# Kernel tuning notes

Hardware: AMD Instinct MI355X
Metric: run time of the kernel (lower is better)

## Reference

```python
import jax, jax.numpy as jnp
import numpy as np

# --- VMO muscle parameters (reconstructed VMOParameters defaults) ---
L0 = 0.089          # optimal_fiber_length [m]
LTS = 0.126         # tendon_slack_length [m]
PENN0 = 0.0873      # pennation_angle_at_optimal [rad]
VMAX = 10.0         # max contraction velocity [optimal lengths / s]
AF = 0.25           # Hill force-velocity curvature
FAT_RATE = 0.01     # fatigue_rate
REC_RATE = 0.002    # recovery_rate
TAU_ACT = 0.01      # activation time constant [s]
TAU_DEACT = 0.04    # deactivation time constant [s]
PHYSICS_WEIGHT = 0.8
LMT_DEFAULT = LTS + L0 * float(np.cos(PENN0))  # default_musculotendon_length
LMIN = 0.5 * L0
LMAX = 1.6 * L0
KT = 35.0           # tendon exponential stiffness
CT = 0.2            # tendon force scale

B, T, H = 8192, 2048, 64


def physics_rhs(state, exc):
    # state: [B, 3] = (fiber_length, activation, fatigue); exc: [B]
    lM = jnp.clip(state[..., 0], LMIN, LMAX)
    act = jnp.clip(state[..., 1], 0.01, 1.0)
    fat = jnp.clip(state[..., 2], 0.0, 1.0)
    a_eff = act * (1.0 - fat)
    # constant-thickness pennation model
    sin_p = jnp.clip(L0 * float(np.sin(PENN0)) / lM, 0.0, 0.99)
    cos_p = jnp.sqrt(1.0 - sin_p * sin_p)
    # Hill-type fiber velocity ODE (elastic tendon, lMT fixed at default, vMT = 0)
    lT = LMT_DEFAULT - lM * cos_p
    epsT = (lT - LTS) / LTS
    fT = jnp.where(epsT > 0.0, CT * (jnp.exp(KT * epsT) - 1.0), 0.0)
    lN = lM / L0
    fL = jnp.exp(-((lN - 1.0) ** 2) / 0.45)
    fPE = jnp.where(lN > 1.0,
                    (jnp.exp(5.0 * (lN - 1.0) / 0.6) - 1.0) / (float(np.exp(5.0)) - 1.0),
                    0.0)
    fV = (fT / cos_p - fPE) / (a_eff * fL + 1e-3)
    vN = jnp.clip((fV - 1.0) / (1.0 + jnp.abs(fV) / AF), -1.0, 1.5)  # inverse force-velocity
    fiber_velocity = VMAX * L0 * vN
    # first-order activation dynamics with activation-dependent time constant
    tau = jnp.where(exc > act, TAU_ACT * (0.5 + 1.5 * act), TAU_DEACT / (0.5 + 1.5 * act))
    activation_dot = (exc - act) / tau
    fatigue_dot = FAT_RATE * a_eff * (1.0 - fat) - REC_RATE * (1.0 - a_eff) * fat
    return jnp.stack([fiber_velocity, activation_dot, fatigue_dot], axis=-1)


def neural_correction(state, exc, W1, b1, W2, b2, W3, b3):
    x = jnp.concatenate([state, exc[..., None]], axis=-1)  # [B, 4]
    h = jnp.tanh(x @ W1 + b1)
    h = jnp.tanh(h @ W2 + b2)
    return 0.1 * jnp.tanh(h @ W3 + b3)


def ode_forward(initial_state, excitation_signal, t_span, W1, b1, W2, b2, W3, b3):
    n = t_span.shape[0]

    def rhs(t, y):
        # piecewise-constant excitation: torch.bucketize(t, t_span) - 1, clamped
        idx = jnp.clip(jnp.searchsorted(t_span, t, side='left') - 1, 0, n - 1)
        exc = excitation_signal[:, idx]
        return physics_rhs(y, exc) + (1.0 - PHYSICS_WEIGHT) * neural_correction(
            y, exc, W1, b1, W2, b2, W3, b3)

    @jax.checkpoint
    def step(y, i):
        t0, t1 = t_span[i], t_span[i + 1]
        dt = t1 - t0
        k1 = rhs(t0, y)
        k2 = rhs(t0 + 0.5 * dt, y + 0.5 * dt * k1)
        k3 = rhs(t0 + 0.5 * dt, y + 0.5 * dt * k2)
        k4 = rhs(t1, y + dt * k3)
        y1 = y + (dt / 6.0) * (k1 + 2.0 * k2 + 2.0 * k3 + k4)
        return y1, y1

    _, ys = jax.lax.scan(step, initial_state, jnp.arange(n - 1))
    return jnp.concatenate([initial_state[None], ys], axis=0)  # [T, B, 3]


def setup_inputs() -> dict:
    key = jax.random.key(0)
    ks = jax.random.split(key, 6)
    lM0 = L0 * (0.8 + 0.4 * jax.random.uniform(ks[0], (B,)))
    a0 = 0.05 + 0.1 * jax.random.uniform(ks[1], (B,))
    initial_state = jnp.stack([lM0, a0, jnp.zeros((B,))], axis=-1).astype(jnp.float32)
    excitation_signal = jax.random.uniform(ks[2], (B, T), dtype=jnp.float32)
    t_span = jnp.linspace(0.0, 2.0, T, dtype=jnp.float32)
    s = 0.1
    W1 = s * jax.random.normal(ks[3], (4, H), dtype=jnp.float32)
    W2 = s * jax.random.normal(ks[4], (H, H), dtype=jnp.float32)
    W3 = s * jax.random.normal(ks[5], (H, 3), dtype=jnp.float32)
    b1 = jnp.zeros((H,), jnp.float32)
    b2 = jnp.zeros((H,), jnp.float32)
    b3 = jnp.zeros((3,), jnp.float32)
    return {"initial_state": initial_state, "excitation_signal": excitation_signal,
            "t_span": t_span, "W1": W1, "b1": b1, "W2": W2, "b2": b2, "W3": W3, "b3": b3}


def reference(initial_state, excitation_signal, t_span, W1, b1, W2, b2, W3, b3):
    return ode_forward(initial_state, excitation_signal, t_span, W1, b1, W2, b2, W3, b3)
```

## Files before the change

kernel.cpp:

```cpp
#include <hip/hip_runtime.h>
#include <cstdint>

#define B_SZ 8192
#define T_SZ 2048

#define C_LTS       0.126f
#define C_LMIN      (0.5f * 0.089f)
#define C_LMAX      (1.6f * 0.089f)
#define C_KT        35.0f
#define C_CT        0.2f
#define C_VMAX_L0   (10.0f * 0.089f)
#define C_AF_INV    4.0f
#define C_FAT_RATE  0.01f
#define C_REC_RATE  0.002f
#define C_TAU_ACT   0.01f
#define C_TAU_DEACT 0.04f
#define C_L0SIN     0.0077598346f
#define C_LMT_DEF   0.2146610680f
#define C_INV_EM5   0.006783655f
#define C_INV_LTS   (1.0f / 0.126f)
#define C_INV_L0    (1.0f / 0.089f)
#define C_NN_SCALE  0.02f

typedef __attribute__((ext_vector_type(8))) short bf16x8;
typedef __attribute__((ext_vector_type(4))) float f32x4;

__device__ __forceinline__ float fast_rcp(float x) { return __builtin_amdgcn_rcpf(x); }
__device__ __forceinline__ float fast_rsq(float x) { return __builtin_amdgcn_rsqf(x); }
__device__ __forceinline__ float fast_tanh(float x) {
    const float e2 = __expf(2.0f * x);
    return 1.0f - 2.0f * fast_rcp(e2 + 1.0f);
}
__device__ __forceinline__ float clampf(float x, float lo, float hi) {
    return fminf(fmaxf(x, lo), hi);
}
__device__ __forceinline__ short f2bf_trunc(float f) {
    return (short)(__float_as_uint(f) >> 16);
}
__device__ __forceinline__ short f2bf_rne(float f) {
    uint32_t u = __float_as_uint(f);
    u += 0x7fff + ((u >> 16) & 1);
    return (short)(u >> 16);
}
__device__ __forceinline__ float bf2f(short s) {
    return __uint_as_float(((uint32_t)(unsigned short)s) << 16);
}

__global__ __launch_bounds__(256) void ode_kernel(
    const float* __restrict__ init_state,
    const float* __restrict__ exc,
    const float* __restrict__ tspan,
    const float* __restrict__ W1,
    const float* __restrict__ b1,
    const float* __restrict__ W2,
    const float* __restrict__ b2,
    const float* __restrict__ W3,
    const float* __restrict__ b3,
    float* __restrict__ out)
{
    const int tid  = threadIdx.x;
    const int wv   = tid >> 6;
    const int lane = tid & 63;
    const int r    = lane & 15;
    const int q    = lane >> 4;
    const int el   = (blockIdx.x << 4) + r;

    __shared__ __align__(16) short h1hi[1024];
    __shared__ __align__(16) short h1lo[1024];
    __shared__ __align__(16) float psum[256];

    float w1r[4][4], b1r[4];
    {
        const int j0 = (wv << 4) + (q << 2);
        #pragma unroll
        for (int u = 0; u < 4; ++u) {
            const int j = j0 + u;
            b1r[u]   = b1[j];
            w1r[0][u] = W1[j];
            w1r[1][u] = W1[64 + j];
            w1r[2][u] = W1[128 + j];
            w1r[3][u] = W1[192 + j];
        }
    }
    const int col = (wv << 4) + r;
    bf16x8 Wh[2], Wl[2];
    #pragma unroll
    for (int ks = 0; ks < 2; ++ks)
        #pragma unroll
        for (int t = 0; t < 8; ++t) {
            const int k = (ks << 5) + (q << 3) + t;
            const float wgt = W2[(k << 6) + col];
            const short hi = f2bf_trunc(wgt);
            Wh[ks][t] = hi;
            Wl[ks][t] = f2bf_rne(wgt - bf2f(hi));
        }
    float b2v4[4], w3r[4][3];
    #pragma unroll
    for (int reg = 0; reg < 4; ++reg) {
        const int c = (wv << 4) + (q << 2) + reg;
        b2v4[reg]  = b2[c];
        w3r[reg][0] = W3[c * 3 + 0];
        w3r[reg][1] = W3[c * 3 + 1];
        w3r[reg][2] = W3[c * 3 + 2];
    }
    const float b3v0 = b3[0], b3v1 = b3[1], b3v2 = b3[2];

    const int slotW = (wv << 1) + (q >> 1);
    const int widx  = (r << 6) + ((slotW ^ (r & 7)) << 3) + ((q & 1) << 2);
    const int ridx0 = (r << 6) + ((q       ^ (r & 7)) << 3);
    const int ridx1 = (r << 6) + (((4 | q) ^ (r & 7)) << 3);
    const int pswidx = (wv << 6) + (r << 2);

    float yb0 = init_state[el * 3 + 0];
    float yb1 = init_state[el * 3 + 1];
    float yb2 = init_state[el * 3 + 2];
    float cs0 = yb0, cs1 = yb1, cs2 = yb2;
    float ka0 = 0.f, ka1 = 0.f, ka2 = 0.f;

    if (wv == 0 && q == 0) {
        out[(size_t)el * 3 + 0] = yb0;
        out[(size_t)el * 3 + 1] = yb1;
        out[(size_t)el * 3 + 2] = yb2;
    }

    const float* excp = exc + (size_t)el * T_SZ;
    float excB = excp[0];
    float excA = excB;
    float tA = tspan[0], tB = tspan[1];

    #pragma unroll 1
    for (int i = 0; i < T_SZ - 1; ++i) {
        const float excN = excp[(i < T_SZ - 2) ? (i + 1) : (T_SZ - 2)];
        const float tN   = tspan[(i <= T_SZ - 3) ? (i + 2) : (T_SZ - 1)];
        const float dt  = tB - tA;
        const float hdt = 0.5f * dt;

        #pragma unroll
        for (int ev = 0; ev < 4; ++ev) {
            const float excv = (ev == 0) ? excA : excB;
            const float s0 = cs0, s1 = cs1, s2 = cs2;

            uint32_t hi01, hi23, lo01, lo23;
            {
                float hv[4];
                #pragma unroll
                for (int u = 0; u < 4; ++u) {
                    float pre = b1r[u];
                    pre = fmaf(s0,   w1r[0][u], pre);
                    pre = fmaf(s1,   w1r[1][u], pre);
                    pre = fmaf(s2,   w1r[2][u], pre);
                    pre = fmaf(excv, w1r[3][u], pre);
                    hv[u] = fast_tanh(pre);
                }
                const unsigned short h0 = (unsigned short)f2bf_trunc(hv[0]);
                const unsigned short h1_ = (unsigned short)f2bf_trunc(hv[1]);
                const unsigned short h2_ = (unsigned short)f2bf_trunc(hv[2]);
                const unsigned short h3_ = (unsigned short)f2bf_trunc(hv[3]);
                hi01 = (uint32_t)h0 | ((uint32_t)h1_ << 16);
                hi23 = (uint32_t)h2_ | ((uint32_t)h3_ << 16);
                const unsigned short l0 = (unsigned short)f2bf_rne(hv[0] - bf2f((short)h0));
                const unsigned short l1 = (unsigned short)f2bf_rne(hv[1] - bf2f((short)h1_));
                const unsigned short l2 = (unsigned short)f2bf_rne(hv[2] - bf2f((short)h2_));
                const unsigned short l3 = (unsigned short)f2bf_rne(hv[3] - bf2f((short)h3_));
                lo01 = (uint32_t)l0 | ((uint32_t)l1 << 16);
                lo23 = (uint32_t)l2 | ((uint32_t)l3 << 16);
            }
            *reinterpret_cast<uint2*>(&h1hi[widx]) = make_uint2(hi01, hi23);
            *reinterpret_cast<uint2*>(&h1lo[widx]) = make_uint2(lo01, lo23);
            __syncthreads();

            const bf16x8 Hh0 = *reinterpret_cast<const bf16x8*>(&h1hi[ridx0]);
            const bf16x8 Hh1 = *reinterpret_cast<const bf16x8*>(&h1hi[ridx1]);
            const bf16x8 Hl0 = *reinterpret_cast<const bf16x8*>(&h1lo[ridx0]);
            const bf16x8 Hl1 = *reinterpret_cast<const bf16x8*>(&h1lo[ridx1]);

            f32x4 accA = {b2v4[0], b2v4[1], b2v4[2], b2v4[3]};
            f32x4 accB = {0.f, 0.f, 0.f, 0.f};
            accA = __builtin_amdgcn_mfma_f32_16x16x32_bf16(Wh[0], Hl0, accA, 0, 0, 0);
            accB = __builtin_amdgcn_mfma_f32_16x16x32_bf16(Wh[1], Hl1, accB, 0, 0, 0);
            accA = __builtin_amdgcn_mfma_f32_16x16x32_bf16(Wl[0], Hh0, accA, 0, 0, 0);
            accB = __builtin_amdgcn_mfma_f32_16x16x32_bf16(Wl[1], Hh1, accB, 0, 0, 0);
            accA = __builtin_amdgcn_mfma_f32_16x16x32_bf16(Wh[0], Hh0, accA, 0, 0, 0);
            accB = __builtin_amdgcn_mfma_f32_16x16x32_bf16(Wh[1], Hh1, accB, 0, 0, 0);

            float p0 = 0.f, p1 = 0.f, p2 = 0.f;
            #pragma unroll
            for (int reg = 0; reg < 4; ++reg) {
                const float h2v = fast_tanh(accA[reg] + accB[reg]);
                p0 = fmaf(h2v, w3r[reg][0], p0);
                p1 = fmaf(h2v, w3r[reg][1], p1);
                p2 = fmaf(h2v, w3r[reg][2], p2);
            }
            p0 += __shfl_xor(p0, 16, 64);
            p1 += __shfl_xor(p1, 16, 64);
            p2 += __shfl_xor(p2, 16, 64);
            p0 += __shfl_xor(p0, 32, 64);
            p1 += __shfl_xor(p1, 32, 64);
            p2 += __shfl_xor(p2, 32, 64);
            if (q == 0) {
                *reinterpret_cast<f32x4*>(&psum[pswidx]) = (f32x4){p0, p1, p2, p2};
            }
            __syncthreads();

            const f32x4 v0 = *reinterpret_cast<const f32x4*>(&psum[(r << 2)]);
            const f32x4 v1 = *reinterpret_cast<const f32x4*>(&psum[64 + (r << 2)]);
            const f32x4 v2 = *reinterpret_cast<const f32x4*>(&psum[128 + (r << 2)]);
            const f32x4 v3 = *reinterpret_cast<const f32x4*>(&psum[192 + (r << 2)]);
            const float S0 = (v0[0] + v1[0]) + (v2[0] + v3[0]);
            const float S1 = (v0[1] + v1[1]) + (v2[1] + v3[1]);
            const float S2 = (v0[2] + v1[2]) + (v2[2] + v3[2]);

            const float nn0 = C_NN_SCALE * fast_tanh(S0 + b3v0);
            const float nn1 = C_NN_SCALE * fast_tanh(S1 + b3v1);
            const float nn2 = C_NN_SCALE * fast_tanh(S2 + b3v2);

            const float lM  = clampf(s0, C_LMIN, C_LMAX);
            const float act = clampf(s1, 0.01f, 1.0f);
            const float fat = clampf(s2, 0.0f, 1.0f);
            const float a_eff = act * (1.0f - fat);
            const float sin_p = fminf(C_L0SIN * fast_rcp(lM), 0.99f);
            const float cp2   = fmaf(-sin_p, sin_p, 1.0f);
            const float inv_cp = fast_rsq(cp2);
            const float cos_p  = cp2 * inv_cp;
            const float lT   = C_LMT_DEF - lM * cos_p;
            const float epsT = (lT - C_LTS) * C_INV_LTS;
            const float fT   = (epsT > 0.0f) ? C_CT * (__expf(C_KT * epsT) - 1.0f) : 0.0f;
            const float lN   = lM * C_INV_L0;
            const float d1   = lN - 1.0f;
            const float fL   = __expf(-d1 * d1 * (1.0f / 0.45f));
            const float fPE  = (lN > 1.0f) ? (__expf(8.3333333333f * d1) - 1.0f) * C_INV_EM5 : 0.0f;
            const float fV   = (fT * inv_cp - fPE) * fast_rcp(fmaf(a_eff, fL, 0.001f));
            float vN = (fV - 1.0f) * fast_rcp(fmaf(fabsf(fV), C_AF_INV, 1.0f));
            vN = clampf(vN, -1.0f, 1.5f);
            const float r0v = fmaf(C_VMAX_L0, vN, nn0);
            const float g15 = fmaf(1.5f, act, 0.5f);
            const float inv_tau = (excv > act) ? fast_rcp(C_TAU_ACT * g15)
                                               : g15 * (1.0f / C_TAU_DEACT);
            const float r1v = fmaf(excv - act, inv_tau, nn1);
            const float r2v = C_FAT_RATE * a_eff * (1.0f - fat)
                            - C_REC_RATE * (1.0f - a_eff) * fat + nn2;

            if (ev == 0) {
                ka0 = r0v; ka1 = r1v; ka2 = r2v;
                cs0 = fmaf(hdt, r0v, yb0); cs1 = fmaf(hdt, r1v, yb1); cs2 = fmaf(hdt, r2v, yb2);
            } else if (ev == 1) {
                ka0 = fmaf(2.0f, r0v, ka0); ka1 = fmaf(2.0f, r1v, ka1); ka2 = fmaf(2.0f, r2v, ka2);
                cs0 = fmaf(hdt, r0v, yb0); cs1 = fmaf(hdt, r1v, yb1); cs2 = fmaf(hdt, r2v, yb2);
            } else if (ev == 2) {
                ka0 = fmaf(2.0f, r0v, ka0); ka1 = fmaf(2.0f, r1v, ka1); ka2 = fmaf(2.0f, r2v, ka2);
                cs0 = fmaf(dt, r0v, yb0); cs1 = fmaf(dt, r1v, yb1); cs2 = fmaf(dt, r2v, yb2);
            } else {
                const float c6 = dt * (1.0f / 6.0f);
                yb0 = fmaf(c6, ka0 + r0v, yb0);
                yb1 = fmaf(c6, ka1 + r1v, yb1);
                yb2 = fmaf(c6, ka2 + r2v, yb2);
                cs0 = yb0; cs1 = yb1; cs2 = yb2;
                if (wv == 0 && q == 0) {
                    const size_t ob = (size_t)(i + 1) * (B_SZ * 3) + (size_t)el * 3;
                    out[ob + 0] = yb0; out[ob + 1] = yb1; out[ob + 2] = yb2;
                }
            }
        }

        excA = excB; excB = excN; tA = tB; tB = tN;
    }
}

extern "C" void kernel_launch(void* const* d_in, const int* in_sizes, int n_in,
                              void* d_out, int out_size, void* d_ws, size_t ws_size,
                              hipStream_t stream) {
    const float* init  = (const float*)d_in[0];
    const float* exc   = (const float*)d_in[1];
    const float* tspan = (const float*)d_in[2];
    const float* W1    = (const float*)d_in[3];
    const float* b1    = (const float*)d_in[4];
    const float* W2    = (const float*)d_in[5];
    const float* b2    = (const float*)d_in[6];
    const float* W3    = (const float*)d_in[7];
    const float* b3    = (const float*)d_in[8];

    hipLaunchKernelGGL(ode_kernel, dim3(B_SZ / 16), dim3(256), 0, stream,
                       init, exc, tspan, W1, b1, W2, b2, W3, b3, (float*)d_out);
}
```

Before: 9.483 ms.

## Process two 16-element batch groups per block to halve barrier count

Each block now handles 32 batch elements as two groups sharing the same barriers and weight registers. Two MFMA chains are issued per stage, and the physics/RK update is split between lane halves, with state exchanged by shuffle. This amortizes __syncthreads and LDS round-trips over twice the work and halves the grid. The costs are 256 blocks instead of 512 (lower occupancy on a large GPU), more registers, and an inner ev loop that is no longer unrolled.

```diff
diff --git a/kernel.cpp b/kernel.cpp
--- a/kernel.cpp
+++ b/kernel.cpp
@@ -63,11 +63,14 @@
     const int lane = tid & 63;
     const int r    = lane & 15;
     const int q    = lane >> 4;
-    const int el   = (blockIdx.x << 4) + r;
-
-    __shared__ __align__(16) short h1hi[1024];
-    __shared__ __align__(16) short h1lo[1024];
-    __shared__ __align__(16) float psum[256];
+    const int gt   = q & 1;
+    const int el0  = (blockIdx.x << 5) + r;
+    const int el1  = el0 + 16;
+    const int el_t = el0 + (gt << 4);
+
+    __shared__ __align__(16) short h1hi[2048];
+    __shared__ __align__(16) short h1lo[2048];
+    __shared__ __align__(16) float psum[512];
 
     float w1r[4][4], b1r[4];
     {
@@ -110,102 +113,123 @@
     const int ridx0 = (r << 6) + ((q       ^ (r & 7)) << 3);
     const int ridx1 = (r << 6) + (((4 | q) ^ (r & 7)) << 3);
     const int pswidx = (wv << 6) + (r << 2);
-
-    float yb0 = init_state[el * 3 + 0];
-    float yb1 = init_state[el * 3 + 1];
-    float yb2 = init_state[el * 3 + 2];
-    float cs0 = yb0, cs1 = yb1, cs2 = yb2;
+    const int prd    = (gt << 8) + (r << 2);
+
+    float cs0_0 = init_state[el0 * 3 + 0];
+    float cs0_1 = init_state[el0 * 3 + 1];
+    float cs0_2 = init_state[el0 * 3 + 2];
+    float cs1_0 = init_state[el1 * 3 + 0];
+    float cs1_1 = init_state[el1 * 3 + 1];
+    float cs1_2 = init_state[el1 * 3 + 2];
+    float yb0 = gt ? cs1_0 : cs0_0;
+    float yb1 = gt ? cs1_1 : cs0_1;
+    float yb2 = gt ? cs1_2 : cs0_2;
     float ka0 = 0.f, ka1 = 0.f, ka2 = 0.f;
 
-    if (wv == 0 && q == 0) {
-        out[(size_t)el * 3 + 0] = yb0;
-        out[(size_t)el * 3 + 1] = yb1;
-        out[(size_t)el * 3 + 2] = yb2;
+    if (wv == 0 && q < 2) {
+        const size_t ob = (size_t)el_t * 3;
+        out[ob + 0] = yb0; out[ob + 1] = yb1; out[ob + 2] = yb2;
     }
 
-    const float* excp = exc + (size_t)el * T_SZ;
-    float excB = excp[0];
-    float excA = excB;
+    const float* excp0 = exc + (size_t)el0 * T_SZ;
+    const float* excp1 = exc + (size_t)el1 * T_SZ;
+    float excB0 = excp0[0], excB1 = excp1[0];
+    float excA0 = excB0,    excA1 = excB1;
     float tA = tspan[0], tB = tspan[1];
 
     #pragma unroll 1
     for (int i = 0; i < T_SZ - 1; ++i) {
-        const float excN = excp[(i < T_SZ - 2) ? (i + 1) : (T_SZ - 2)];
-        const float tN   = tspan[(i <= T_SZ - 3) ? (i + 2) : (T_SZ - 1)];
+        const int ip = (i < T_SZ - 2) ? (i + 1) : (T_SZ - 2);
+        const float excN0 = excp0[ip];
+        const float excN1 = excp1[ip];
+        const float tN    = tspan[(i <= T_SZ - 3) ? (i + 2) : (T_SZ - 1)];
         const float dt  = tB - tA;
         const float hdt = 0.5f * dt;
 
-        #pragma unroll
+        #pragma unroll 1
         for (int ev = 0; ev < 4; ++ev) {
-            const float excv = (ev == 0) ? excA : excB;
-            const float s0 = cs0, s1 = cs1, s2 = cs2;
-
-            uint32_t hi01, hi23, lo01, lo23;
-            {
+            const float excv0 = (ev == 0) ? excA0 : excB0;
+            const float excv1 = (ev == 0) ? excA1 : excB1;
+
+            #pragma unroll
+            for (int g = 0; g < 2; ++g) {
+                const float s0 = g ? cs1_0 : cs0_0;
+                const float s1 = g ? cs1_1 : cs0_1;
+                const float s2 = g ? cs1_2 : cs0_2;
+                const float ex = g ? excv1 : excv0;
                 float hv[4];
                 #pragma unroll
                 for (int u = 0; u < 4; ++u) {
                     float pre = b1r[u];
-                    pre = fmaf(s0,   w1r[0][u], pre);
-                    pre = fmaf(s1,   w1r[1][u], pre);
-                    pre = fmaf(s2,   w1r[2][u], pre);
-                    pre = fmaf(excv, w1r[3][u], pre);
+                    pre = fmaf(s0, w1r[0][u], pre);
+                    pre = fmaf(s1, w1r[1][u], pre);
+                    pre = fmaf(s2, w1r[2][u], pre);
+                    pre = fmaf(ex, w1r[3][u], pre);
                     hv[u] = fast_tanh(pre);
                 }
                 const unsigned short h0 = (unsigned short)f2bf_trunc(hv[0]);
                 const unsigned short h1_ = (unsigned short)f2bf_trunc(hv[1]);
                 const unsigned short h2_ = (unsigned short)f2bf_trunc(hv[2]);
                 const unsigned short h3_ = (unsigned short)f2bf_trunc(hv[3]);
-                hi01 = (uint32_t)h0 | ((uint32_t)h1_ << 16);
-                hi23 = (uint32_t)h2_ | ((uint32_t)h3_ << 16);
+                const uint32_t hi01 = (uint32_t)h0 | ((uint32_t)h1_ << 16);
+                const uint32_t hi23 = (uint32_t)h2_ | ((uint32_t)h3_ << 16);
                 const unsigned short l0 = (unsigned short)f2bf_rne(hv[0] - bf2f((short)h0));
                 const unsigned short l1 = (unsigned short)f2bf_rne(hv[1] - bf2f((short)h1_));
                 const unsigned short l2 = (unsigned short)f2bf_rne(hv[2] - bf2f((short)h2_));
                 const unsigned short l3 = (unsigned short)f2bf_rne(hv[3] - bf2f((short)h3_));
-                lo01 = (uint32_t)l0 | ((uint32_t)l1 << 16);
-                lo23 = (uint32_t)l2 | ((uint32_t)l3 << 16);
-            }
-            *reinterpret_cast<uint2*>(&h1hi[widx]) = make_uint2(hi01, hi23);
-            *reinterpret_cast<uint2*>(&h1lo[widx]) = make_uint2(lo01, lo23);
-            __syncthreads();
-
-            const bf16x8 Hh0 = *reinterpret_cast<const bf16x8*>(&h1hi[ridx0]);
-            const bf16x8 Hh1 = *reinterpret_cast<const bf16x8*>(&h1hi[ridx1]);
-            const bf16x8 Hl0 = *reinterpret_cast<const bf16x8*>(&h1lo[ridx0]);
-            const bf16x8 Hl1 = *reinterpret_cast<const bf16x8*>(&h1lo[ridx1]);
-
-            f32x4 accA = {b2v4[0], b2v4[1], b2v4[2], b2v4[3]};
-            f32x4 accB = {0.f, 0.f, 0.f, 0.f};
-            accA = __builtin_amdgcn_mfma_f32_16x16x32_bf16(Wh[0], Hl0, accA, 0, 0, 0);
-            accB = __builtin_amdgcn_mfma_f32_16x16x32_bf16(Wh[1], Hl1, accB, 0, 0, 0);
-            accA = __builtin_amdgcn_mfma_f32_16x16x32_bf16(Wl[0], Hh0, accA, 0, 0, 0);
-            accB = __builtin_amdgcn_mfma_f32_16x16x32_bf16(Wl[1], Hh1, accB, 0, 0, 0);
-            accA = __builtin_amdgcn_mfma_f32_16x16x32_bf16(Wh[0], Hh0, accA, 0, 0, 0);
-            accB = __builtin_amdgcn_mfma_f32_16x16x32_bf16(Wh[1], Hh1, accB, 0, 0, 0);
-
-            float p0 = 0.f, p1 = 0.f, p2 = 0.f;
-            #pragma unroll
-            for (int reg = 0; reg < 4; ++reg) {
-                const float h2v = fast_tanh(accA[reg] + accB[reg]);
-                p0 = fmaf(h2v, w3r[reg][0], p0);
-                p1 = fmaf(h2v, w3r[reg][1], p1);
-                p2 = fmaf(h2v, w3r[reg][2], p2);
-            }
-            p0 += __shfl_xor(p0, 16, 64);
-            p1 += __shfl_xor(p1, 16, 64);
-            p2 += __shfl_xor(p2, 16, 64);
-            p0 += __shfl_xor(p0, 32, 64);
-            p1 += __shfl_xor(p1, 32, 64);
-            p2 += __shfl_xor(p2, 32, 64);
-            if (q == 0) {
-                *reinterpret_cast<f32x4*>(&psum[pswidx]) = (f32x4){p0, p1, p2, p2};
+                const uint32_t lo01 = (uint32_t)l0 | ((uint32_t)l1 << 16);
+                const uint32_t lo23 = (uint32_t)l2 | ((uint32_t)l3 << 16);
+                const int o = g << 10;
+                *reinterpret_cast<uint2*>(&h1hi[widx + o]) = make_uint2(hi01, hi23);
+                *reinterpret_cast<uint2*>(&h1lo[widx + o]) = make_uint2(lo01, lo23);
             }
             __syncthreads();
 
-            const f32x4 v0 = *reinterpret_cast<const f32x4*>(&psum[(r << 2)]);
-            const f32x4 v1 = *reinterpret_cast<const f32x4*>(&psum[64 + (r << 2)]);
-            const f32x4 v2 = *reinterpret_cast<const f32x4*>(&psum[128 + (r << 2)]);
-            const f32x4 v3 = *reinterpret_cast<const f32x4*>(&psum[192 + (r << 2)]);
+            f32x4 accA[2], accB[2];
+            #pragma unroll
+            for (int g = 0; g < 2; ++g) {
+                const int o = g << 10;
+                const bf16x8 Hh0 = *reinterpret_cast<const bf16x8*>(&h1hi[ridx0 + o]);
+                const bf16x8 Hh1 = *reinterpret_cast<const bf16x8*>(&h1hi[ridx1 + o]);
+                const bf16x8 Hl0 = *reinterpret_cast<const bf16x8*>(&h1lo[ridx0 + o]);
+                const bf16x8 Hl1 = *reinterpret_cast<const bf16x8*>(&h1lo[ridx1 + o]);
+                accA[g] = (f32x4){b2v4[0], b2v4[1], b2v4[2], b2v4[3]};
+                accB[g] = (f32x4){0.f, 0.f, 0.f, 0.f};
+                accA[g] = __builtin_amdgcn_mfma_f32_16x16x32_bf16(Wh[0], Hl0, accA[g], 0, 0, 0);
+                accB[g] = __builtin_amdgcn_mfma_f32_16x16x32_bf16(Wh[1], Hl1, accB[g], 0, 0, 0);
+                accA[g] = __builtin_amdgcn_mfma_f32_16x16x32_bf16(Wl[0], Hh0, accA[g], 0, 0, 0);
+                accB[g] = __builtin_amdgcn_mfma_f32_16x16x32_bf16(Wl[1], Hh1, accB[g], 0, 0, 0);
+                accA[g] = __builtin_amdgcn_mfma_f32_16x16x32_bf16(Wh[0], Hh0, accA[g], 0, 0, 0);
+                accB[g] = __builtin_amdgcn_mfma_f32_16x16x32_bf16(Wh[1], Hh1, accB[g], 0, 0, 0);
+            }
+
+            #pragma unroll
+            for (int g = 0; g < 2; ++g) {
+                float p0 = 0.f, p1 = 0.f, p2 = 0.f;
+                #pragma unroll
+                for (int reg = 0; reg < 4; ++reg) {
+                    const float h2v = fast_tanh(accA[g][reg] + accB[g][reg]);
+                    p0 = fmaf(h2v, w3r[reg][0], p0);
+                    p1 = fmaf(h2v, w3r[reg][1], p1);
+                    p2 = fmaf(h2v, w3r[reg][2], p2);
+                }
+                p0 += __shfl_xor(p0, 16, 64);
+                p1 += __shfl_xor(p1, 16, 64);
+                p2 += __shfl_xor(p2, 16, 64);
+                p0 += __shfl_xor(p0, 32, 64);
+                p1 += __shfl_xor(p1, 32, 64);
+                p2 += __shfl_xor(p2, 32, 64);
+                if (q == 0) {
+                    *reinterpret_cast<f32x4*>(&psum[(g << 8) + pswidx]) =
+                        (f32x4){p0, p1, p2, p2};
+                }
+            }
+            __syncthreads();
+
+            const f32x4 v0 = *reinterpret_cast<const f32x4*>(&psum[prd]);
+            const f32x4 v1 = *reinterpret_cast<const f32x4*>(&psum[prd + 64]);
+            const f32x4 v2 = *reinterpret_cast<const f32x4*>(&psum[prd + 128]);
+            const f32x4 v3 = *reinterpret_cast<const f32x4*>(&psum[prd + 192]);
             const float S0 = (v0[0] + v1[0]) + (v2[0] + v3[0]);
             const float S1 = (v0[1] + v1[1]) + (v2[1] + v3[1]);
             const float S2 = (v0[2] + v1[2]) + (v2[2] + v3[2]);
@@ -214,9 +238,14 @@
             const float nn1 = C_NN_SCALE * fast_tanh(S1 + b3v1);
             const float nn2 = C_NN_SCALE * fast_tanh(S2 + b3v2);
 
-            const float lM  = clampf(s0, C_LMIN, C_LMAX);
-            const float act = clampf(s1, 0.01f, 1.0f);
-            const float fat = clampf(s2, 0.0f, 1.0f);
+            const float ts0 = gt ? cs1_0 : cs0_0;
+            const float ts1 = gt ? cs1_1 : cs0_1;
+            const float ts2 = gt ? cs1_2 : cs0_2;
+            const float tex = gt ? excv1 : excv0;
+
+            const float lM  = clampf(ts0, C_LMIN, C_LMAX);
+            const float act = clampf(ts1, 0.01f, 1.0f);
+            const float fat = clampf(ts2, 0.0f, 1.0f);
             const float a_eff = act * (1.0f - fat);
             const float sin_p = fminf(C_L0SIN * fast_rcp(lM), 0.99f);
             const float cp2   = fmaf(-sin_p, sin_p, 1.0f);
@@ -234,35 +263,45 @@
             vN = clampf(vN, -1.0f, 1.5f);
             const float r0v = fmaf(C_VMAX_L0, vN, nn0);
             const float g15 = fmaf(1.5f, act, 0.5f);
-            const float inv_tau = (excv > act) ? fast_rcp(C_TAU_ACT * g15)
-                                               : g15 * (1.0f / C_TAU_DEACT);
-            const float r1v = fmaf(excv - act, inv_tau, nn1);
+            const float inv_tau = (tex > act) ? fast_rcp(C_TAU_ACT * g15)
+                                              : g15 * (1.0f / C_TAU_DEACT);
+            const float r1v = fmaf(tex - act, inv_tau, nn1);
             const float r2v = C_FAT_RATE * a_eff * (1.0f - fat)
                             - C_REC_RATE * (1.0f - a_eff) * fat + nn2;
 
+            float ns0, ns1, ns2;
             if (ev == 0) {
                 ka0 = r0v; ka1 = r1v; ka2 = r2v;
-                cs0 = fmaf(hdt, r0v, yb0); cs1 = fmaf(hdt, r1v, yb1); cs2 = fmaf(hdt, r2v, yb2);
+                ns0 = fmaf(hdt, r0v, yb0); ns1 = fmaf(hdt, r1v, yb1); ns2 = fmaf(hdt, r2v, yb2);
             } else if (ev == 1) {
                 ka0 = fmaf(2.0f, r0v, ka0); ka1 = fmaf(2.0f, r1v, ka1); ka2 = fmaf(2.0f, r2v, ka2);
-                cs0 = fmaf(hdt, r0v, yb0); cs1 = fmaf(hdt, r1v, yb1); cs2 = fmaf(hdt, r2v, yb2);
+                ns0 = fmaf(hdt, r0v, yb0); ns1 = fmaf(hdt, r1v, yb1); ns2 = fmaf(hdt, r2v, yb2);
             } else if (ev == 2) {
                 ka0 = fmaf(2.0f, r0v, ka0); ka1 = fmaf(2.0f, r1v, ka1); ka2 = fmaf(2.0f, r2v, ka2);
-                cs0 = fmaf(dt, r0v, yb0); cs1 = fmaf(dt, r1v, yb1); cs2 = fmaf(dt, r2v, yb2);
+                ns0 = fmaf(dt, r0v, yb0); ns1 = fmaf(dt, r1v, yb1); ns2 = fmaf(dt, r2v, yb2);
             } else {
                 const float c6 = dt * (1.0f / 6.0f);
                 yb0 = fmaf(c6, ka0 + r0v, yb0);
                 yb1 = fmaf(c6, ka1 + r1v, yb1);
                 yb2 = fmaf(c6, ka2 + r2v, yb2);
-                cs0 = yb0; cs1 = yb1; cs2 = yb2;
-                if (wv == 0 && q == 0) {
-                    const size_t ob = (size_t)(i + 1) * (B_SZ * 3) + (size_t)el * 3;
-                    out[ob + 0] = yb0; out[ob + 1] = yb1; out[ob + 2] = yb2;
+                ns0 = yb0; ns1 = yb1; ns2 = yb2;
+                if (wv == 0 && q < 2) {
+                    const size_t ob = (size_t)(i + 1) * (B_SZ * 3) + (size_t)el_t * 3;
+                    out[ob + 0] = ns0; out[ob + 1] = ns1; out[ob + 2] = ns2;
                 }
             }
+
+            const float sw0 = __shfl_xor(ns0, 16, 64);
+            const float sw1 = __shfl_xor(ns1, 16, 64);
+            const float sw2 = __shfl_xor(ns2, 16, 64);
+            cs0_0 = gt ? sw0 : ns0;  cs1_0 = gt ? ns0 : sw0;
+            cs0_1 = gt ? sw1 : ns1;  cs1_1 = gt ? ns1 : sw1;
+            cs0_2 = gt ? sw2 : ns2;  cs1_2 = gt ? ns2 : sw2;
         }
 
-        excA = excB; excB = excN; tA = tB; tB = tN;
+        excA0 = excB0; excB0 = excN0;
+        excA1 = excB1; excB1 = excN1;
+        tA = tB; tB = tN;
     }
 }
 
@@ -279,6 +318,6 @@
     const float* W3    = (const float*)d_in[7];
     const float* b3    = (const float*)d_in[8];
 
-    hipLaunchKernelGGL(ode_kernel, dim3(B_SZ / 16), dim3(256), 0, stream,
+    hipLaunchKernelGGL(ode_kernel, dim3(B_SZ / 32), dim3(256), 0, stream,
                        init, exc, tspan, W1, b1, W2, b2, W3, b3, (float*)d_out);
 }
```

Result: slower. 10.56 ms (+11.3%).
